# Kernel tuning notes

Hardware: AMD Instinct MI355X
Metric: run time of the kernel (lower is better)

## Reference

```python
import jax, jax.numpy as jnp
import numpy as np
from jax import lax

N = 50000      # num_nodes
D = 128        # hidden_dim
P = 6          # num_path
L1 = 6         # path_length1
L2 = 4         # path_length2


def setup_inputs() -> dict:
    key = jax.random.key(0)
    k1, k2, k3, k4, k5, k6 = jax.random.split(key, 6)
    feats = jax.random.normal(k1, (N, D), dtype=jnp.float32)
    init_feats = jax.random.normal(k2, (N, D), dtype=jnp.float32)
    paths = jax.random.randint(k3, (P, N, L1), 0, N, dtype=jnp.int64)
    # xavier_normal with gain=1.414 for (1, L, D): std = gain*sqrt(2/(L+D)) on fan dims of last two axes
    std1 = 1.414 * np.sqrt(2.0 / (L1 + D))
    std2 = 1.414 * np.sqrt(2.0 / (L2 + D))
    std_fc = 1.414 * np.sqrt(2.0 / (D + D))
    path_weight1 = jax.random.normal(k4, (1, L1, D), dtype=jnp.float32) * std1
    path_weight2 = jax.random.normal(k5, (1, L2, D), dtype=jnp.float32) * std2
    fc_weight = jax.random.normal(k6, (D, D), dtype=jnp.float32) * std_fc  # Linear weight (out, in)
    return {
        "feats": feats,
        "paths": paths,
        "init_feats": init_feats,
        "flag": 1,
        "path_weight1": path_weight1,
        "path_weight2": path_weight2,
        "fc_weight": fc_weight,
    }


def reference(feats, paths, init_feats, flag, path_weight1, path_weight2, fc_weight):
    # flag is a Python int constant selecting which path-weight bank to use
    w = path_weight1[0] if flag == 1 else path_weight2[0]  # (L, D)
    num_path = paths.shape[0]

    def body(acc, p):
        # p: (N, L) node indices; gather (N, L, D), weighted-sum over path dim
        pf = feats[p]                       # (N, L, D)
        acc = acc + jnp.einsum("nld,ld->nd", pf, w)
        return acc, None

    acc, _ = lax.scan(body, jnp.zeros((feats.shape[0], feats.shape[1]), feats.dtype), paths)
    results = acc / num_path
    out = jax.nn.relu(results @ fc_weight.T)  # Linear(bias=False): x @ W^T
    return out
```

## Files before the change

### kernel.cpp

```cpp
#include <hip/hip_runtime.h>
#include <stdint.h>

#define NN 50000
#define DD 128
#define PP 6
#define LL 6
#define GN 64
#define WPAD 136

typedef float f4 __attribute__((ext_vector_type(4)));
typedef short bf16x8 __attribute__((ext_vector_type(8)));

__device__ __forceinline__ uint16_t f2bf(float f) {
  uint32_t u = __float_as_uint(f);
  u = (u + 0x7fffu + ((u >> 16) & 1u)) >> 16;
  return (uint16_t)u;
}
__device__ __forceinline__ float bf_lo(uint32_t u) { return __uint_as_float(u << 16); }
__device__ __forceinline__ float bf_hi(uint32_t u) { return __uint_as_float(u & 0xffff0000u); }

__global__ __launch_bounds__(256) void k_cvt(const float* __restrict__ in,
                                             uint16_t* __restrict__ out, int n4) {
  int i = blockIdx.x * 256 + threadIdx.x;
  if (i >= n4) return;
  f4 v = ((const f4*)in)[i];
  ushort4 o;
  o.x = f2bf(v.x); o.y = f2bf(v.y); o.z = f2bf(v.z); o.w = f2bf(v.w);
  ((ushort4*)out)[i] = o;
}

__global__ __launch_bounds__(256) void k_gather(
    const uint16_t* __restrict__ fb,
    const int* __restrict__ paths,
    const float* __restrict__ w,
    uint16_t* __restrict__ accb) {
  __shared__ int sidx[PP * GN * LL];
  const int t = threadIdx.x;
  const int nb = blockIdx.x * GN;

  #pragma unroll
  for (int s = 0; s < 9; ++s) {
    const int i = s * 256 + t;
    const int p = i / (GN * LL);
    const int rem = i - p * (GN * LL);
    const long g = (long)nb * LL + rem;
    int val = 0;
    if (g < (long)NN * LL) val = paths[(size_t)p * NN * LL + g];
    sidx[i] = val;
  }

  const int lane = t & 31;
  const int grp  = t >> 5;
  const int d0   = lane * 4;

  const float sc = 1.f / 6.f;
  f4 wl[LL];
  #pragma unroll
  for (int l = 0; l < LL; ++l) {
    f4 v = *(const f4*)(w + l * DD + d0);
    wl[l].x = v.x * sc; wl[l].y = v.y * sc; wl[l].z = v.z * sc; wl[l].w = v.w * sc;
  }

  __syncthreads();

  #pragma unroll 1
  for (int s = 0; s < 8; ++s) {
    const int ni = grp * 8 + s;
    const int n = nb + ni;
    uint2 v[PP * LL];
    #pragma unroll
    for (int p = 0; p < PP; ++p)
      #pragma unroll
      for (int l = 0; l < LL; ++l) {
        const int idx = sidx[(p * GN + ni) * LL + l];
        v[p * LL + l] = *(const uint2*)(fb + (size_t)idx * DD + d0);
      }
    f4 a = {0.f, 0.f, 0.f, 0.f};
    #pragma unroll
    for (int p = 0; p < PP; ++p)
      #pragma unroll
      for (int l = 0; l < LL; ++l) {
        const uint2 u = v[p * LL + l];
        a.x = fmaf(wl[l].x, bf_lo(u.x), a.x);
        a.y = fmaf(wl[l].y, bf_hi(u.x), a.y);
        a.z = fmaf(wl[l].z, bf_lo(u.y), a.z);
        a.w = fmaf(wl[l].w, bf_hi(u.y), a.w);
      }
    if (n < NN) {
      ushort4 o;
      o.x = f2bf(a.x); o.y = f2bf(a.y); o.z = f2bf(a.z); o.w = f2bf(a.w);
      *(ushort4*)(accb + (size_t)n * DD + d0) = o;
    }
  }
}

__global__ __launch_bounds__(256) void k_fc(
    const uint16_t* __restrict__ accb,
    const float* __restrict__ fcw,
    float* __restrict__ out) {
  __shared__ uint16_t sA[64 * WPAD];
  __shared__ uint16_t sW[128 * WPAD];
  const int t = threadIdx.x;
  const int nb = blockIdx.x * 64;

  #pragma unroll
  for (int it = 0; it < 4; ++it) {
    const int chunk = it * 256 + t;
    const int row = chunk >> 4, c8 = chunk & 15;
    uint4 v = {0u, 0u, 0u, 0u};
    if (nb + row < NN) v = *(const uint4*)(accb + (size_t)(nb + row) * DD + c8 * 8);
    *(uint4*)(sA + row * WPAD + c8 * 8) = v;
  }
  #pragma unroll
  for (int it = 0; it < 16; ++it) {
    const int chunk = it * 256 + t;
    const int row = chunk >> 5, c4 = chunk & 31;
    f4 v = *(const f4*)(fcw + row * DD + c4 * 4);
    ushort4 o;
    o.x = f2bf(v.x); o.y = f2bf(v.y); o.z = f2bf(v.z); o.w = f2bf(v.w);
    *(ushort4*)(sW + row * WPAD + c4 * 4) = o;
  }
  __syncthreads();

  const int w  = t >> 6;
  const int l  = t & 63;
  const int lr = l & 15;
  const int hk = (l >> 4) * 8;

  bf16x8 afrag[4];
  #pragma unroll
  for (int k0 = 0; k0 < 4; ++k0)
    afrag[k0] = *(bf16x8*)(sA + (w * 16 + lr) * WPAD + k0 * 32 + hk);

  #pragma unroll
  for (int o = 0; o < 8; ++o) {
    f4 dacc = {0.f, 0.f, 0.f, 0.f};
    #pragma unroll
    for (int k0 = 0; k0 < 4; ++k0) {
      bf16x8 bfrag = *(bf16x8*)(sW + (o * 16 + lr) * WPAD + k0 * 32 + hk);
      dacc = __builtin_amdgcn_mfma_f32_16x16x32_bf16(afrag[k0], bfrag, dacc, 0, 0, 0);
    }
    const int col = o * 16 + lr;
    #pragma unroll
    for (int r = 0; r < 4; ++r) {
      const int n = nb + w * 16 + (l >> 4) * 4 + r;
      if (n < NN) out[(size_t)n * DD + col] = fmaxf(dacc[r], 0.f);
    }
  }
}

extern "C" void kernel_launch(void* const* d_in, const int* in_sizes, int n_in,
                              void* d_out, int out_size, void* d_ws, size_t ws_size,
                              hipStream_t stream) {
  const float* feats = (const float*)d_in[0];
  const int*   paths = (const int*)d_in[1];
  const float* pw1   = (const float*)d_in[4];
  const float* fcw   = (const float*)d_in[6];
  float* out = (float*)d_out;

  uint16_t* fb   = (uint16_t*)d_ws;
  uint16_t* accb = (uint16_t*)((char*)d_ws + (size_t)NN * DD * 2);

  const int n4 = NN * DD / 4;
  k_cvt<<<(n4 + 255) / 256, 256, 0, stream>>>(feats, fb, n4);
  k_gather<<<(NN + GN - 1) / GN, 256, 0, stream>>>(fb, paths, pw1, accb);
  k_fc<<<(NN + 63) / 64, 256, 0, stream>>>(accb, fcw, out);
}
```

Measured before the change: 82.40 us.

## Fuse path gather and FC matmul into one kernel via shared memory

Merges the gather/weighted-sum kernel with the FC MFMA kernel so the bf16 per-node accumulator stays in LDS instead of round-tripping through global memory. The fc weight conversion to bf16 moves into the conversion kernel, so each gather block only copies pre-converted weights into LDS. This removes one launch and the intermediate write and read. In exchange, LDS per block grows by about 52KB, which may cut occupancy for the latency-bound gather phase.

```diff
diff --git a/kernel.cpp b/kernel.cpp
--- a/kernel.cpp
+++ b/kernel.cpp
@@ -19,22 +19,31 @@
 __device__ __forceinline__ float bf_lo(uint32_t u) { return __uint_as_float(u << 16); }
 __device__ __forceinline__ float bf_hi(uint32_t u) { return __uint_as_float(u & 0xffff0000u); }
 
-__global__ __launch_bounds__(256) void k_cvt(const float* __restrict__ in,
-                                             uint16_t* __restrict__ out, int n4) {
+__global__ __launch_bounds__(256) void k_cvt(const float* __restrict__ feats,
+                                             const float* __restrict__ fcw,
+                                             uint16_t* __restrict__ fb,
+                                             uint16_t* __restrict__ wb,
+                                             int n4, int w4) {
   int i = blockIdx.x * 256 + threadIdx.x;
-  if (i >= n4) return;
-  f4 v = ((const f4*)in)[i];
+  const float* src; uint16_t* dst; int j;
+  if (i < n4)            { src = feats; dst = fb; j = i; }
+  else if (i < n4 + w4)  { src = fcw;   dst = wb; j = i - n4; }
+  else return;
+  f4 v = ((const f4*)src)[j];
   ushort4 o;
   o.x = f2bf(v.x); o.y = f2bf(v.y); o.z = f2bf(v.z); o.w = f2bf(v.w);
-  ((ushort4*)out)[i] = o;
+  ((ushort4*)dst)[j] = o;
 }
 
-__global__ __launch_bounds__(256) void k_gather(
+__global__ __launch_bounds__(256) void k_gfc(
     const uint16_t* __restrict__ fb,
     const int* __restrict__ paths,
     const float* __restrict__ w,
-    uint16_t* __restrict__ accb) {
+    const uint16_t* __restrict__ wb,
+    float* __restrict__ out) {
   __shared__ int sidx[PP * GN * LL];
+  __shared__ uint16_t sA[GN * WPAD];
+  __shared__ uint16_t sW[DD * WPAD];
   const int t = threadIdx.x;
   const int nb = blockIdx.x * GN;
 
@@ -47,6 +56,13 @@
     int val = 0;
     if (g < (long)NN * LL) val = paths[(size_t)p * NN * LL + g];
     sidx[i] = val;
+  }
+  #pragma unroll
+  for (int it = 0; it < 8; ++it) {
+    const int chunk = it * 256 + t;
+    const int row = chunk >> 4, c8 = chunk & 15;
+    uint4 v = *(const uint4*)(wb + (size_t)row * DD + c8 * 8);
+    *(uint4*)(sW + row * WPAD + c8 * 8) = v;
   }
 
   const int lane = t & 31;
@@ -66,7 +82,6 @@
   #pragma unroll 1
   for (int s = 0; s < 8; ++s) {
     const int ni = grp * 8 + s;
-    const int n = nb + ni;
     uint2 v[PP * LL];
     #pragma unroll
     for (int p = 0; p < PP; ++p)
@@ -86,43 +101,14 @@
         a.z = fmaf(wl[l].z, bf_lo(u.y), a.z);
         a.w = fmaf(wl[l].w, bf_hi(u.y), a.w);
       }
-    if (n < NN) {
-      ushort4 o;
-      o.x = f2bf(a.x); o.y = f2bf(a.y); o.z = f2bf(a.z); o.w = f2bf(a.w);
-      *(ushort4*)(accb + (size_t)n * DD + d0) = o;
-    }
+    ushort4 o;
+    o.x = f2bf(a.x); o.y = f2bf(a.y); o.z = f2bf(a.z); o.w = f2bf(a.w);
+    *(ushort4*)(sA + ni * WPAD + d0) = o;
   }
-}
 
-__global__ __launch_bounds__(256) void k_fc(
-    const uint16_t* __restrict__ accb,
-    const float* __restrict__ fcw,
-    float* __restrict__ out) {
-  __shared__ uint16_t sA[64 * WPAD];
-  __shared__ uint16_t sW[128 * WPAD];
-  const int t = threadIdx.x;
-  const int nb = blockIdx.x * 64;
-
-  #pragma unroll
-  for (int it = 0; it < 4; ++it) {
-    const int chunk = it * 256 + t;
-    const int row = chunk >> 4, c8 = chunk & 15;
-    uint4 v = {0u, 0u, 0u, 0u};
-    if (nb + row < NN) v = *(const uint4*)(accb + (size_t)(nb + row) * DD + c8 * 8);
-    *(uint4*)(sA + row * WPAD + c8 * 8) = v;
-  }
-  #pragma unroll
-  for (int it = 0; it < 16; ++it) {
-    const int chunk = it * 256 + t;
-    const int row = chunk >> 5, c4 = chunk & 31;
-    f4 v = *(const f4*)(fcw + row * DD + c4 * 4);
-    ushort4 o;
-    o.x = f2bf(v.x); o.y = f2bf(v.y); o.z = f2bf(v.z); o.w = f2bf(v.w);
-    *(ushort4*)(sW + row * WPAD + c4 * 4) = o;
-  }
   __syncthreads();
 
-  const int w  = t >> 6;
+  const int wv = t >> 6;
   const int l  = t & 63;
   const int lr = l & 15;
   const int hk = (l >> 4) * 8;
@@ -130,7 +116,7 @@
   bf16x8 afrag[4];
   #pragma unroll
   for (int k0 = 0; k0 < 4; ++k0)
-    afrag[k0] = *(bf16x8*)(sA + (w * 16 + lr) * WPAD + k0 * 32 + hk);
+    afrag[k0] = *(bf16x8*)(sA + (wv * 16 + lr) * WPAD + k0 * 32 + hk);
 
   #pragma unroll
   for (int o = 0; o < 8; ++o) {
@@ -143,7 +129,7 @@
     const int col = o * 16 + lr;
     #pragma unroll
     for (int r = 0; r < 4; ++r) {
-      const int n = nb + w * 16 + (l >> 4) * 4 + r;
+      const int n = nb + wv * 16 + (l >> 4) * 4 + r;
       if (n < NN) out[(size_t)n * DD + col] = fmaxf(dacc[r], 0.f);
     }
   }
@@ -158,11 +144,11 @@
   const float* fcw   = (const float*)d_in[6];
   float* out = (float*)d_out;
 
-  uint16_t* fb   = (uint16_t*)d_ws;
-  uint16_t* accb = (uint16_t*)((char*)d_ws + (size_t)NN * DD * 2);
+  uint16_t* fb = (uint16_t*)d_ws;
+  uint16_t* wb = (uint16_t*)((char*)d_ws + (size_t)NN * DD * 2);
 
   const int n4 = NN * DD / 4;
-  k_cvt<<<(n4 + 255) / 256, 256, 0, stream>>>(feats, fb, n4);
-  k_gather<<<(NN + GN - 1) / GN, 256, 0, stream>>>(fb, paths, pw1, accb);
-  k_fc<<<(NN + 63) / 64, 256, 0, stream>>>(accb, fcw, out);
+  const int w4 = DD * DD / 4;
+  k_cvt<<<(n4 + w4 + 255) / 256, 256, 0, stream>>>(feats, fcw, fb, wb, n4, w4);
+  k_gfc<<<(NN + GN - 1) / GN, 256, 0, stream>>>(fb, paths, pw1, wb, out);
 }
```

Measured after the change: 76.20 us. -7.5%, faster.
